# Kernel tuning notes

Hardware: AMD Instinct MI355X
Metric: run time of the kernel (lower is better)

The kernel has to match this reference:

```python
import jax, jax.numpy as jnp
import numpy as np

P = 16          # patch size (square)
HEADS = 8
DH = 64         # dim per head
SCALE = DH ** -0.5
EPS = 1e-5


def layernorm(x, g, b):
    mu = x.mean(-1, keepdims=True)
    var = ((x - mu) ** 2).mean(-1, keepdims=True)
    return (x - mu) * jax.lax.rsqrt(var + EPS) * g + b


def sattn(q, k, v):
    # q:[..., i, d], k/v:[..., j, d]; q already scaled
    sim = jnp.einsum('...id,...jd->...ij', q, k)
    a = jax.nn.softmax(sim, axis=-1)
    return jnp.einsum('...ij,...jd->...id', a, v)


def split_heads(t, b, N):
    return t.reshape(b, N, HEADS, DH).transpose(0, 2, 1, 3).reshape(b * HEADS, N, DH)


def merge_heads(t, b, N):
    return t.reshape(b, HEADS, N, DH).transpose(0, 2, 1, 3).reshape(b, N, HEADS * DH)


def qkv_cls(x, ln_g, ln_b, qkv_w):
    b, N, _ = x.shape
    xn = layernorm(x, ln_g, ln_b)
    q, k, v = jnp.split(xn @ qkv_w, 3, axis=-1)
    q = split_heads(q, b, N) * SCALE
    k = split_heads(k, b, N)
    v = split_heads(v, b, N)
    cls_out = sattn(q[:, :1], k, v)          # cls attends to everything
    return q[:, 1:], k[:, 1:], v[:, 1:], k[:, :1], v[:, :1], cls_out


def time_attention(x, ln_g, ln_b, qkv_w, out_w, out_b, f, n):
    b, N, _ = x.shape
    q_, k_, v_, cls_k, cls_v, cls_out = qkv_cls(x, ln_g, ln_b, qkv_w)
    bh = b * HEADS
    resh = lambda t: t.reshape(bh, f, n, DH).transpose(0, 2, 1, 3)  # 'b (f n) d -> (b n) f d' kept as [bh,n,f,d]
    q_, k_, v_ = resh(q_), resh(k_), resh(v_)
    ck = jnp.broadcast_to(cls_k[:, None], (bh, n, 1, DH))
    cv = jnp.broadcast_to(cls_v[:, None], (bh, n, 1, DH))
    out = sattn(q_, jnp.concatenate([ck, k_], 2), jnp.concatenate([cv, v_], 2))
    out = out.transpose(0, 2, 1, 3).reshape(bh, f * n, DH)
    out = jnp.concatenate([cls_out, out], axis=1)
    return merge_heads(out, b, N) @ out_w + out_b


def space_attention(x, ln_g, ln_b, qkv_w, out_w, out_b, f, n):
    b, N, _ = x.shape
    q_, k_, v_, cls_k, cls_v, cls_out = qkv_cls(x, ln_g, ln_b, qkv_w)
    bh = b * HEADS
    resh = lambda t: t.reshape(bh, f, n, DH)  # 'b (f n) d -> (b f) n d' kept as [bh,f,n,d]
    q_, k_, v_ = resh(q_), resh(k_), resh(v_)
    m = n // 2
    ck = jnp.broadcast_to(cls_k[:, None], (bh, f, 1, DH))
    cv = jnp.broadcast_to(cls_v[:, None], (bh, f, 1, DH))
    # mutual attention: first half queries attend to [cls, second half], and vice versa
    out1 = sattn(q_[:, :, :m], jnp.concatenate([ck, k_[:, :, m:]], 2), jnp.concatenate([cv, v_[:, :, m:]], 2))
    out2 = sattn(q_[:, :, m:], jnp.concatenate([ck, k_[:, :, :m]], 2), jnp.concatenate([cv, v_[:, :, :m]], 2))
    out = jnp.concatenate([out1, out2], axis=2).reshape(bh, f * n, DH)
    out = jnp.concatenate([cls_out, out], axis=1)
    return merge_heads(out, b, N) @ out_w + out_b


def geglu_ff(x, ln_g, ln_b, w1, b1, w2, b2):
    xn = layernorm(x, ln_g, ln_b)
    h = xn @ w1 + b1
    u, g = jnp.split(h, 2, axis=-1)
    return (u * jax.nn.gelu(g, approximate=False)) @ w2 + b2


def setup_inputs() -> dict:
    key = jax.random.key(0)
    ks = jax.random.split(key, 12)
    D, DEPTH, NC = 512, 12, 60
    inner = HEADS * DH
    B, F, C, H, W = 1, 4, 3, 480, 640
    n = (H // P) * (W // P)        # 1200
    N = F * n + 1                  # 4801
    pd = C * P * P                 # 768
    s = 0.02
    rn = lambda k, sh: jax.random.normal(k, sh, jnp.float32) * s
    z = lambda sh: jnp.zeros(sh, jnp.float32)
    o = lambda sh: jnp.ones(sh, jnp.float32)
    return {
        'video': jax.random.normal(ks[0], (B, F, C, H, W), jnp.float32),
        'patch_w': rn(ks[1], (pd, D)), 'patch_b': z((D,)),
        'pos_emb': rn(ks[2], (N, D)),
        'cls_token': rn(ks[3], (1, D)),
        't_ln_g': o((DEPTH, D)), 't_ln_b': z((DEPTH, D)),
        't_qkv_w': rn(ks[4], (DEPTH, D, 3 * inner)),
        't_out_w': rn(ks[5], (DEPTH, inner, D)), 't_out_b': z((DEPTH, D)),
        's_ln_g': o((DEPTH, D)), 's_ln_b': z((DEPTH, D)),
        's_qkv_w': rn(ks[6], (DEPTH, D, 3 * inner)),
        's_out_w': rn(ks[7], (DEPTH, inner, D)), 's_out_b': z((DEPTH, D)),
        'f_ln_g': o((DEPTH, D)), 'f_ln_b': z((DEPTH, D)),
        'f_w1': rn(ks[8], (DEPTH, D, 8 * D)), 'f_b1': z((DEPTH, 8 * D)),
        'f_w2': rn(ks[9], (DEPTH, 4 * D, D)), 'f_b2': z((DEPTH, D)),
        'o_ln_g': o((D,)), 'o_ln_b': z((D,)),
        'o_w': rn(ks[10], (D, NC)), 'o_b': z((NC,)),
    }


def reference(video, patch_w, patch_b, pos_emb, cls_token,
              t_ln_g, t_ln_b, t_qkv_w, t_out_w, t_out_b,
              s_ln_g, s_ln_b, s_qkv_w, s_out_w, s_out_b,
              f_ln_g, f_ln_b, f_w1, f_b1, f_w2, f_b2,
              o_ln_g, o_ln_b, o_w, o_b):
    b, f, c, H, W = video.shape
    hh, ww = H // P, W // P
    n = hh * ww
    wh = ww // 2
    half = W // 2

    def patchify(v):  # v: [b,f,c,H,W/2] -> [b, f*hh*wh, P*P*c]
        v = v.reshape(b, f, c, hh, P, wh, P)
        v = v.transpose(0, 1, 3, 5, 4, 6, 2)  # b f h w p1 p2 c
        return v.reshape(b, f * hh * wh, P * P * c)

    tok = jnp.concatenate([patchify(video[..., :half]), patchify(video[..., half:])], axis=1)
    tok = tok @ patch_w + patch_b
    x = jnp.concatenate([jnp.broadcast_to(cls_token[None], (b, 1, tok.shape[-1])), tok], axis=1)
    x = x + pos_emb[: x.shape[1]]

    depth = t_qkv_w.shape[0]
    for i in range(depth):
        x = time_attention(x, t_ln_g[i], t_ln_b[i], t_qkv_w[i], t_out_w[i], t_out_b[i], f, n) + x
        x = space_attention(x, s_ln_g[i], s_ln_b[i], s_qkv_w[i], s_out_w[i], s_out_b[i], f, n) + x
        x = geglu_ff(x, f_ln_g[i], f_ln_b[i], f_w1[i], f_b1[i], f_w2[i], f_b2[i]) + x

    cls = layernorm(x[:, 0], o_ln_g, o_ln_b)
    return cls @ o_w + o_b
```

## Files before the change

kernel.cpp:

```cpp
#include <hip/hip_runtime.h>
#include <cmath>


#define NT      4801
#define NP      4800
#define MP      4864
#define DM      512
#define QKV_ST  1536
#define LN_EPS  1e-5f
#define NCH     49

typedef __attribute__((ext_vector_type(8))) short bf16x8;
typedef __attribute__((ext_vector_type(4))) float f32x4;

__device__ __forceinline__ unsigned short f2b(float f) {
    union { float f; unsigned int u; } x; x.f = f;
    unsigned int r = (x.u + 0x7FFFu + ((x.u >> 16) & 1u)) >> 16;
    return (unsigned short)r;
}
__device__ __forceinline__ float b2f(unsigned short b) {
    union { unsigned int u; float f; } x; x.u = ((unsigned int)b) << 16;
    return x.f;
}
__device__ __forceinline__ unsigned int pack2(float a, float b) {
    return (unsigned int)f2b(a) | ((unsigned int)f2b(b) << 16);
}

__device__ __forceinline__ void gl_lds16(const void* g, void* l) {
    __builtin_amdgcn_global_load_lds(
        (__attribute__((address_space(1))) unsigned int*)(unsigned long long)(uintptr_t)g,
        (__attribute__((address_space(3))) unsigned int*)l, 16, 0, 0);
}

__global__ void patchify_kernel(const float* __restrict__ video, unsigned short* __restrict__ out)
{
    int idx = blockIdx.x * 256 + threadIdx.x;
    if (idx >= NP * 768) return;
    int tok = idx / 768, e = idx % 768;
    int c  = e % 3;
    int pe = e / 3;
    int p2 = pe % 16, p1 = pe / 16;
    int half = tok / 2400, r = tok % 2400;
    int f = r / 600, rr = r % 600;
    int hi = rr / 20, wi = rr % 20;
    int row = hi * 16 + p1;
    int col = half * 320 + wi * 16 + p2;
    out[idx] = f2b(video[(((size_t)f * 3 + c) * 480 + row) * 640 + col]);
}

__global__ void cls_init_kernel(const float* __restrict__ cls_token,
                                const float* __restrict__ pos, float* __restrict__ X)
{
    int d = blockIdx.x * 256 + threadIdx.x;
    if (d < DM) X[d] = cls_token[d] + pos[d];
}

__device__ __forceinline__ void transpose_tile(const float* __restrict__ in,
                                               unsigned short* __restrict__ out,
                                               int K, int N, int tile)
{
    __shared__ float T[32][33];
    int ntk = K / 32;
    int kt = tile % ntk, nt = tile / ntk;
    int k0 = kt * 32, n0 = nt * 32;
    int tx = threadIdx.x & 31, ty = threadIdx.x >> 5;
    #pragma unroll
    for (int i = 0; i < 4; i++)
        T[ty + 8 * i][tx] = in[(size_t)(k0 + ty + 8 * i) * N + n0 + tx];
    __syncthreads();
    #pragma unroll
    for (int i = 0; i < 4; i++)
        out[(size_t)(n0 + ty + 8 * i) * K + k0 + tx] = f2b(T[tx][ty + 8 * i]);
}

__global__ __launch_bounds__(256) void convertT_layer(
    const float* __restrict__ w0, const float* __restrict__ w1,
    const float* __restrict__ w2, const float* __restrict__ w3,
    const float* __restrict__ w4, const float* __restrict__ w5,
    unsigned short* __restrict__ out)
{
    int t = blockIdx.x;
    if      (t <  768) transpose_tile(w0, out + 0,       512, 1536, t);
    else if (t < 1024) transpose_tile(w1, out + 786432,  512,  512, t - 768);
    else if (t < 1792) transpose_tile(w2, out + 1048576, 512, 1536, t - 1024);
    else if (t < 2048) transpose_tile(w3, out + 1835008, 512,  512, t - 1792);
    else if (t < 4096) transpose_tile(w4, out + 2097152, 512, 4096, t - 2048);
    else               transpose_tile(w5, out + 4194304, 2048, 512, t - 4096);
}

__global__ __launch_bounds__(256) void convertT_one(
    const float* __restrict__ in, unsigned short* __restrict__ out, int K, int N)
{
    transpose_tile(in, out, K, N, blockIdx.x);
}

template<bool OB16>
__global__ __launch_bounds__(256, 4) void mfma_gemm(
    const unsigned short* __restrict__ A, const unsigned short* __restrict__ BT,
    const float* __restrict__ bias, const float* __restrict__ add,
    void* __restrict__ C, int Mv, int N, int K)
{
    __shared__ short Asm[128 * 64];
    __shared__ short Bsm[128 * 64];
    const int tid = threadIdx.x, w = tid >> 6, lane = tid & 63;
    const int row0 = blockIdx.y * 128, col0 = blockIdx.x * 128;
    const int wm = w >> 1, wn = w & 1;
    const int l15 = lane & 15, quad = lane >> 4;

    f32x4 acc[4][4] = {};

    int arows[4], aqs[4];
    #pragma unroll
    for (int i = 0; i < 4; i++) {
        int s = (w * 4 + i) * 64 + lane;
        arows[i] = s >> 3;
        aqs[i]   = (s & 7) ^ ((s >> 3) & 7);
    }

    for (int k0 = 0; k0 < K; k0 += 64) {
        __syncthreads();
        #pragma unroll
        for (int i = 0; i < 4; i++) {
            gl_lds16(A  + (size_t)(row0 + arows[i]) * K + k0 + aqs[i] * 8,
                     &Asm[(w * 4 + i) * 512]);
            gl_lds16(BT + (size_t)(col0 + arows[i]) * K + k0 + aqs[i] * 8,
                     &Bsm[(w * 4 + i) * 512]);
        }
        __syncthreads();
        #pragma unroll
        for (int ks = 0; ks < 2; ks++) {
            bf16x8 af[4], bfr[4];
            #pragma unroll
            for (int i = 0; i < 4; i++) {
                int m  = wm * 64 + i * 16 + l15;
                int pa = (ks * 4 + quad) ^ (m & 7);
                af[i]  = *(const bf16x8*)&Asm[m * 64 + pa * 8];
                int n  = wn * 64 + i * 16 + l15;
                int pb = (ks * 4 + quad) ^ (n & 7);
                bfr[i] = *(const bf16x8*)&Bsm[n * 64 + pb * 8];
            }
            #pragma unroll
            for (int i = 0; i < 4; i++)
                #pragma unroll
                for (int j = 0; j < 4; j++)
                    acc[i][j] = __builtin_amdgcn_mfma_f32_16x16x32_bf16(
                                    af[i], bfr[j], acc[i][j], 0, 0, 0);
        }
    }

    #pragma unroll
    for (int i = 0; i < 4; i++) {
        #pragma unroll
        for (int r = 0; r < 4; r++) {
            int row = row0 + wm * 64 + i * 16 + quad * 4 + r;
            if (row >= Mv) continue;
            #pragma unroll
            for (int j = 0; j < 4; j++) {
                int col = col0 + wn * 64 + j * 16 + l15;
                float v = acc[i][j][r];
                if (bias) v += bias[col];
                if (add)  v += add[(size_t)row * N + col];
                if (OB16) ((unsigned short*)C)[(size_t)row * N + col] = f2b(v);
                else      ((float*)C)[(size_t)row * N + col] = v;
            }
        }
    }
}

template<int SPLITS>
__global__ __launch_bounds__(256, 4) void mfma_gemm_sk(
    const unsigned short* __restrict__ A, const unsigned short* __restrict__ BT,
    const float* __restrict__ bias, float* __restrict__ C, int Mv, int N, int K)
{
    __shared__ short Asm[128 * 64];
    __shared__ short Bsm[128 * 64];
    const int tid = threadIdx.x, w = tid >> 6, lane = tid & 63;
    const int row0 = blockIdx.y * 128, col0 = blockIdx.x * 128;
    const int wm = w >> 1, wn = w & 1;
    const int l15 = lane & 15, quad = lane >> 4;
    const int kchunk = K / SPLITS;
    const int kbeg = blockIdx.z * kchunk;

    f32x4 acc[4][4] = {};

    int arows[4], aqs[4];
    #pragma unroll
    for (int i = 0; i < 4; i++) {
        int s = (w * 4 + i) * 64 + lane;
        arows[i] = s >> 3;
        aqs[i]   = (s & 7) ^ ((s >> 3) & 7);
    }

    for (int k0 = kbeg; k0 < kbeg + kchunk; k0 += 64) {
        __syncthreads();
        #pragma unroll
        for (int i = 0; i < 4; i++) {
            gl_lds16(A  + (size_t)(row0 + arows[i]) * K + k0 + aqs[i] * 8,
                     &Asm[(w * 4 + i) * 512]);
            gl_lds16(BT + (size_t)(col0 + arows[i]) * K + k0 + aqs[i] * 8,
                     &Bsm[(w * 4 + i) * 512]);
        }
        __syncthreads();
        #pragma unroll
        for (int ks = 0; ks < 2; ks++) {
            bf16x8 af[4], bfr[4];
            #pragma unroll
            for (int i = 0; i < 4; i++) {
                int m  = wm * 64 + i * 16 + l15;
                int pa = (ks * 4 + quad) ^ (m & 7);
                af[i]  = *(const bf16x8*)&Asm[m * 64 + pa * 8];
                int n  = wn * 64 + i * 16 + l15;
                int pb = (ks * 4 + quad) ^ (n & 7);
                bfr[i] = *(const bf16x8*)&Bsm[n * 64 + pb * 8];
            }
            #pragma unroll
            for (int i = 0; i < 4; i++)
                #pragma unroll
                for (int j = 0; j < 4; j++)
                    acc[i][j] = __builtin_amdgcn_mfma_f32_16x16x32_bf16(
                                    af[i], bfr[j], acc[i][j], 0, 0, 0);
        }
    }

    const bool addb = (blockIdx.z == 0) && (bias != nullptr);
    #pragma unroll
    for (int i = 0; i < 4; i++) {
        #pragma unroll
        for (int r = 0; r < 4; r++) {
            int row = row0 + wm * 64 + i * 16 + quad * 4 + r;
            if (row >= Mv) continue;
            #pragma unroll
            for (int j = 0; j < 4; j++) {
                int col = col0 + wn * 64 + j * 16 + l15;
                float v = acc[i][j][r];
                if (addb) v += bias[col];
                unsafeAtomicAdd(&C[(size_t)row * N + col], v);
            }
        }
    }
}

__global__ __launch_bounds__(256) void ln_bf16(
    const float* __restrict__ x, const float* __restrict__ g,
    const float* __restrict__ b, unsigned short* __restrict__ y, int M)
{
    int wid = threadIdx.x >> 6, lane = threadIdx.x & 63;
    int row = blockIdx.x * 4 + wid;
    if (row >= M) return;
    const float4* xr = (const float4*)(x + (size_t)row * DM);
    float4 v0 = xr[lane * 2], v1 = xr[lane * 2 + 1];
    float s  = v0.x + v0.y + v0.z + v0.w + v1.x + v1.y + v1.z + v1.w;
    float s2 = v0.x*v0.x + v0.y*v0.y + v0.z*v0.z + v0.w*v0.w
             + v1.x*v1.x + v1.y*v1.y + v1.z*v1.z + v1.w*v1.w;
    #pragma unroll
    for (int off = 32; off >= 1; off >>= 1) {
        s  += __shfl_xor(s, off);
        s2 += __shfl_xor(s2, off);
    }
    float mu = s * (1.f / DM);
    float var = s2 * (1.f / DM) - mu * mu;
    float r = rsqrtf(var + LN_EPS);
    const float4* gv = (const float4*)g;
    const float4* bv = (const float4*)b;
    unsigned int* yr = (unsigned int*)(y + (size_t)row * DM);
    #pragma unroll
    for (int i = 0; i < 2; i++) {
        float4 v = (i == 0) ? v0 : v1;
        float4 gg = gv[lane * 2 + i], bb = bv[lane * 2 + i];
        float ox = (v.x - mu) * r * gg.x + bb.x;
        float oy = (v.y - mu) * r * gg.y + bb.y;
        float oz = (v.z - mu) * r * gg.z + bb.z;
        float ow = (v.w - mu) * r * gg.w + bb.w;
        yr[lane * 4 + i * 2 + 0] = pack2(ox, oy);
        yr[lane * 4 + i * 2 + 1] = pack2(oz, ow);
    }
}

__global__ __launch_bounds__(256, 2) void time_attn(
    const unsigned short* __restrict__ qkv, unsigned short* __restrict__ out)
{
    int t = blockIdx.x * 256 + threadIdx.x;
    if (t >= 8 * NP) return;
    int h = t / NP, j = t - h * NP;
    int pos = j % 1200;
    union { bf16x8 v; unsigned short u[8]; } ld;
    float q[64];
    const unsigned short* qp = qkv + (size_t)(j + 1) * QKV_ST + h * 64;
    #pragma unroll
    for (int c = 0; c < 8; c++) {
        ld.v = *(const bf16x8*)(qp + c * 8);
        #pragma unroll
        for (int e = 0; e < 8; e++) q[c * 8 + e] = b2f(ld.u[e]) * 0.125f;
    }
    int rows[5] = {0, pos + 1, pos + 1201, pos + 2401, pos + 3601};
    float s[5];
    #pragma unroll
    for (int kk = 0; kk < 5; kk++) {
        const unsigned short* kp = qkv + (size_t)rows[kk] * QKV_ST + 512 + h * 64;
        float ss = 0.f;
        #pragma unroll
        for (int c = 0; c < 8; c++) {
            ld.v = *(const bf16x8*)(kp + c * 8);
            #pragma unroll
            for (int e = 0; e < 8; e++) ss += q[c * 8 + e] * b2f(ld.u[e]);
        }
        s[kk] = ss;
    }
    float mx = s[0];
    #pragma unroll
    for (int kk = 1; kk < 5; kk++) mx = fmaxf(mx, s[kk]);
    float e5[5], l = 0.f;
    #pragma unroll
    for (int kk = 0; kk < 5; kk++) { e5[kk] = __expf(s[kk] - mx); l += e5[kk]; }
    float rl = 1.f / l;
    float acc[64];
    #pragma unroll
    for (int d = 0; d < 64; d++) acc[d] = 0.f;
    #pragma unroll
    for (int kk = 0; kk < 5; kk++) {
        float p = e5[kk] * rl;
        const unsigned short* vp = qkv + (size_t)rows[kk] * QKV_ST + 1024 + h * 64;
        #pragma unroll
        for (int c = 0; c < 8; c++) {
            ld.v = *(const bf16x8*)(vp + c * 8);
            #pragma unroll
            for (int e = 0; e < 8; e++) acc[c * 8 + e] += p * b2f(ld.u[e]);
        }
    }
    unsigned int* op = (unsigned int*)(out + (size_t)(j + 1) * DM + h * 64);
    #pragma unroll
    for (int d2 = 0; d2 < 32; d2++) op[d2] = pack2(acc[2 * d2], acc[2 * d2 + 1]);
}

#define SPAD 72
__global__ __launch_bounds__(256, 2) void space_attn_mfma(
    const unsigned short* __restrict__ qkv, unsigned short* __restrict__ out)
{
    __shared__ short Ksm[64 * SPAD];
    __shared__ short VTsm[64 * SPAD];
    __shared__ short Psm[4][32 * SPAD];
    int qt = blockIdx.x, h = blockIdx.y, g = blockIdx.z;
    int f = g >> 1, half = g & 1;
    int tid = threadIdx.x, w = tid >> 6, lane = tid & 63;
    int l15 = lane & 15, quad = lane >> 4;

    int qrow_base = qt * 128 + w * 32;
    int qb = 1 + f * 1200 + half * 600;
    int kb = 1 + f * 1200 + (1 - half) * 600;

    bf16x8 aQ[2][2];
    #pragma unroll
    for (int mf = 0; mf < 2; mf++) {
        int qr = qrow_base + mf * 16 + l15;
        int qtok = qb + ((qr < 600) ? qr : 0);
        const unsigned short* qp = qkv + (size_t)qtok * QKV_ST + h * 64;
        #pragma unroll
        for (int ks = 0; ks < 2; ks++)
            aQ[mf][ks] = *(const bf16x8*)(qp + ks * 32 + quad * 8);
    }

    f32x4 O[2][4] = {};
    float mrow[2][4], lrow[2][4];
    #pragma unroll
    for (int mf = 0; mf < 2; mf++)
        #pragma unroll
        for (int r = 0; r < 4; r++) { mrow[mf][r] = -1e30f; lrow[mf][r] = 0.f; }

    for (int kt = 0; kt < 10; kt++) {
        __syncthreads();
        #pragma unroll
        for (int it = 0; it < 2; it++) {
            int c = tid + it * 256;
            int row = c >> 3, dc = (c & 7) * 8;
            int kidx = kt * 64 + row;
            int tok = (kidx == 0) ? 0 : ((kidx <= 600) ? kb + kidx - 1 : 0);
            const unsigned short* kp = qkv + (size_t)tok * QKV_ST + 512 + h * 64 + dc;
            *(bf16x8*)&Ksm[row * SPAD + dc] = *(const bf16x8*)kp;
            union { bf16x8 v; unsigned short u[8]; } vv;
            vv.v = *(const bf16x8*)(kp + 512);
            #pragma unroll
            for (int e = 0; e < 8; e++)
                VTsm[(dc + e) * SPAD + row] = vv.u[e];
        }
        __syncthreads();

        f32x4 S[2][4] = {};
        #pragma unroll
        for (int ks = 0; ks < 2; ks++) {
            bf16x8 bK[4];
            #pragma unroll
            for (int nf = 0; nf < 4; nf++)
                bK[nf] = *(const bf16x8*)&Ksm[(nf * 16 + l15) * SPAD + ks * 32 + quad * 8];
            #pragma unroll
            for (int mf = 0; mf < 2; mf++)
                #pragma unroll
                for (int nf = 0; nf < 4; nf++)
                    S[mf][nf] = __builtin_amdgcn_mfma_f32_16x16x32_bf16(
                                    aQ[mf][ks], bK[nf], S[mf][nf], 0, 0, 0);
        }

        #pragma unroll
        for (int mf = 0; mf < 2; mf++) {
            float pv[4][4];
            float lm[4] = {-1e30f, -1e30f, -1e30f, -1e30f};
            #pragma unroll
            for (int nf = 0; nf < 4; nf++) {
                int kidx = kt * 64 + nf * 16 + l15;
                bool valid = kidx <= 600;
                #pragma unroll
                for (int r = 0; r < 4; r++) {
                    float s = valid ? S[mf][nf][r] * 0.125f : -1e30f;
                    pv[nf][r] = s;
                    lm[r] = fmaxf(lm[r], s);
                }
            }
            #pragma unroll
            for (int off = 1; off < 16; off <<= 1)
                #pragma unroll
                for (int r = 0; r < 4; r++)
                    lm[r] = fmaxf(lm[r], __shfl_xor(lm[r], off));
            #pragma unroll
            for (int r = 0; r < 4; r++) {
                float nm = fmaxf(mrow[mf][r], lm[r]);
                float c = __expf(mrow[mf][r] - nm);
                mrow[mf][r] = nm;
                lrow[mf][r] *= c;
                #pragma unroll
                for (int nf = 0; nf < 4; nf++) O[mf][nf][r] *= c;
            }
            float rs[4] = {0.f, 0.f, 0.f, 0.f};
            #pragma unroll
            for (int nf = 0; nf < 4; nf++)
                #pragma unroll
                for (int r = 0; r < 4; r++) {
                    float p = __expf(pv[nf][r] - mrow[mf][r]);
                    pv[nf][r] = p;
                    rs[r] += p;
                }
            #pragma unroll
            for (int off = 1; off < 16; off <<= 1)
                #pragma unroll
                for (int r = 0; r < 4; r++)
                    rs[r] += __shfl_xor(rs[r], off);
            #pragma unroll
            for (int r = 0; r < 4; r++) lrow[mf][r] += rs[r];
            #pragma unroll
            for (int nf = 0; nf < 4; nf++)
                #pragma unroll
                for (int r = 0; r < 4; r++)
                    Psm[w][(mf * 16 + quad * 4 + r) * SPAD + nf * 16 + l15] = (short)f2b(pv[nf][r]);
        }
        asm volatile("s_waitcnt lgkmcnt(0)" ::: "memory");

        #pragma unroll
        for (int ks2 = 0; ks2 < 2; ks2++) {
            bf16x8 aP[2], bV[4];
            #pragma unroll
            for (int mf = 0; mf < 2; mf++)
                aP[mf] = *(const bf16x8*)&Psm[w][(mf * 16 + l15) * SPAD + ks2 * 32 + quad * 8];
            #pragma unroll
            for (int nf = 0; nf < 4; nf++)
                bV[nf] = *(const bf16x8*)&VTsm[(nf * 16 + l15) * SPAD + ks2 * 32 + quad * 8];
            #pragma unroll
            for (int mf = 0; mf < 2; mf++)
                #pragma unroll
                for (int nf = 0; nf < 4; nf++)
                    O[mf][nf] = __builtin_amdgcn_mfma_f32_16x16x32_bf16(
                                    aP[mf], bV[nf], O[mf][nf], 0, 0, 0);
        }
    }

    #pragma unroll
    for (int mf = 0; mf < 2; mf++)
        #pragma unroll
        for (int r = 0; r < 4; r++) {
            int qr = qrow_base + mf * 16 + quad * 4 + r;
            if (qr >= 600) continue;
            int qtok = qb + qr;
            float rl = 1.f / lrow[mf][r];
            #pragma unroll
            for (int nf = 0; nf < 4; nf++)
                out[(size_t)qtok * DM + h * 64 + nf * 16 + l15] = f2b(O[mf][nf][r] * rl);
        }
}

__global__ __launch_bounds__(256) void cls_attn_part(
    const unsigned short* __restrict__ qkv, float* __restrict__ part)
{
    int ch = blockIdx.x, h = blockIdx.y;
    int wid = threadIdx.x >> 6, lane = threadIdx.x & 63;
    __shared__ float sm[4], sl[4], sa[4][64];
    float qv = b2f(qkv[h * 64 + lane]) * 0.125f;
    int k0 = ch * 100 + wid * 25;
    float m = -1e30f, l = 0.f, acc = 0.f;
    for (int i = 0; i < 25; i += 2) {
        int key0 = k0 + i, key1 = key0 + 1;
        bool ok0 = key0 < NT;
        bool ok1 = (i + 1 < 25) && (key1 < NT);
        const unsigned short* kr0 = qkv + (size_t)(ok0 ? key0 : 0) * QKV_ST + 512 + h * 64;
        const unsigned short* kr1 = qkv + (size_t)(ok1 ? key1 : 0) * QKV_ST + 512 + h * 64;
        float s0 = qv * b2f(kr0[lane]);
        float v0 = b2f(kr0[512 + lane]);
        float s1 = qv * b2f(kr1[lane]);
        float v1 = b2f(kr1[512 + lane]);
        #pragma unroll
        for (int off = 32; off >= 1; off >>= 1) {
            s0 += __shfl_xor(s0, off);
            s1 += __shfl_xor(s1, off);
        }
        float nm = m;
        if (ok0) nm = fmaxf(nm, s0);
        if (ok1) nm = fmaxf(nm, s1);
        float c  = __expf(m - nm);
        float p0 = ok0 ? __expf(s0 - nm) : 0.f;
        float p1 = ok1 ? __expf(s1 - nm) : 0.f;
        l   = l * c + p0 + p1;
        acc = acc * c + p0 * v0 + p1 * v1;
        m = nm;
    }
    if (lane == 0) { sm[wid] = m; sl[wid] = l; }
    sa[wid][lane] = acc;
    __syncthreads();
    if (wid == 0) {
        float M2 = fmaxf(fmaxf(sm[0], sm[1]), fmaxf(sm[2], sm[3]));
        float L = 0.f, o = 0.f;
        #pragma unroll
        for (int w = 0; w < 4; w++) {
            float c = __expf(sm[w] - M2);
            L += sl[w] * c;
            o += sa[w][lane] * c;
        }
        float* p = part + ((size_t)h * NCH + ch) * 68;
        if (lane == 0) { p[0] = M2; p[1] = L; }
        p[4 + lane] = o;
    }
}

__global__ __launch_bounds__(64) void cls_attn_reduce(
    const float* __restrict__ part, unsigned short* __restrict__ out)
{
    int h = blockIdx.x, lane = threadIdx.x;
    float m = -1e30f, l = 0.f, acc = 0.f;
    for (int c = 0; c < NCH; c++) {
        const float* p = part + ((size_t)h * NCH + c) * 68;
        float cm = p[0], cl = p[1], ca = p[4 + lane];
        float nm = fmaxf(m, cm);
        float e1 = __expf(m - nm), e2 = __expf(cm - nm);
        l   = l * e1 + cl * e2;
        acc = acc * e1 + ca * e2;
        m = nm;
    }
    out[h * 64 + lane] = f2b(acc / l);
}

__global__ __launch_bounds__(256) void geglu_kernel(
    const unsigned short* __restrict__ h, unsigned short* __restrict__ out)
{
    int idx = blockIdx.x * 256 + threadIdx.x;
    if (idx >= NT * 256) return;
    int r = idx >> 8, cc = (idx & 255) * 8;
    const unsigned short* up = h + (size_t)r * 4096 + cc;
    const unsigned short* gp = up + 2048;
    float o[8];
    #pragma unroll
    for (int e = 0; e < 8; e++) {
        float u = b2f(up[e]), gg = b2f(gp[e]);
        o[e] = u * 0.5f * gg * (1.f + erff(gg * 0.70710678f));
    }
    unsigned int* op = (unsigned int*)(out + (size_t)r * 2048 + cc);
    #pragma unroll
    for (int e = 0; e < 4; e++) op[e] = pack2(o[2 * e], o[2 * e + 1]);
}

__global__ __launch_bounds__(64) void head_kernel(
    const float* __restrict__ x, const float* __restrict__ g,
    const float* __restrict__ b, const float* __restrict__ w,
    const float* __restrict__ ob, float* __restrict__ out)
{
    __shared__ float xn[DM];
    int lane = threadIdx.x;
    const float4* xr = (const float4*)x;
    float4 v0 = xr[lane * 2], v1 = xr[lane * 2 + 1];
    float s  = v0.x + v0.y + v0.z + v0.w + v1.x + v1.y + v1.z + v1.w;
    float s2 = v0.x*v0.x + v0.y*v0.y + v0.z*v0.z + v0.w*v0.w
             + v1.x*v1.x + v1.y*v1.y + v1.z*v1.z + v1.w*v1.w;
    #pragma unroll
    for (int off = 32; off >= 1; off >>= 1) {
        s  += __shfl_xor(s, off);
        s2 += __shfl_xor(s2, off);
    }
    float mu = s * (1.f / DM);
    float var = s2 * (1.f / DM) - mu * mu;
    float r = rsqrtf(var + LN_EPS);
    #pragma unroll
    for (int i = 0; i < 8; i++) {
        int d = lane * 8 + i;
        xn[d] = (x[d] - mu) * r * g[d] + b[d];
    }
    __syncthreads();
    if (lane < 60) {
        float a = ob[lane];
        for (int d = 0; d < DM; d++) a += xn[d] * w[d * 60 + lane];
        out[lane] = a;
    }
}

extern "C" void kernel_launch(void* const* d_in, const int* in_sizes, int n_in,
                              void* d_out, int out_size, void* d_ws, size_t ws_size,
                              hipStream_t stream)
{
    const float* video     = (const float*)d_in[0];
    const float* patch_w   = (const float*)d_in[1];
    const float* patch_b   = (const float*)d_in[2];
    const float* pos_emb   = (const float*)d_in[3];
    const float* cls_token = (const float*)d_in[4];
    const float* t_ln_g    = (const float*)d_in[5];
    const float* t_ln_b    = (const float*)d_in[6];
    const float* t_qkv_w   = (const float*)d_in[7];
    const float* t_out_w   = (const float*)d_in[8];
    const float* t_out_b   = (const float*)d_in[9];
    const float* s_ln_g    = (const float*)d_in[10];
    const float* s_ln_b    = (const float*)d_in[11];
    const float* s_qkv_w   = (const float*)d_in[12];
    const float* s_out_w   = (const float*)d_in[13];
    const float* s_out_b   = (const float*)d_in[14];
    const float* f_ln_g    = (const float*)d_in[15];
    const float* f_ln_b    = (const float*)d_in[16];
    const float* f_w1      = (const float*)d_in[17];
    const float* f_b1      = (const float*)d_in[18];
    const float* f_w2      = (const float*)d_in[19];
    const float* f_b2      = (const float*)d_in[20];
    const float* o_ln_g    = (const float*)d_in[21];
    const float* o_ln_b    = (const float*)d_in[22];
    const float* o_w       = (const float*)d_in[23];
    const float* o_b       = (const float*)d_in[24];

    char* ws = (char*)d_ws;
    size_t o = 0;
    float*          X    = (float*)(ws + o);          o += (size_t)(MP + 1) * 512 * 4;
    unsigned short* XN   = (unsigned short*)(ws + o); o += (size_t)MP * 512 * 2;
    unsigned short* QKV  = (unsigned short*)(ws + o); o += (size_t)MP * 1536 * 2;
    unsigned short* H16  = (unsigned short*)(ws + o); o += (size_t)MP * 4096 * 2;
    unsigned short* MID  = (unsigned short*)(ws + o); o += (size_t)MP * 2048 * 2;
    unsigned short* PT   = (unsigned short*)(ws + o); o += (size_t)MP * 768 * 2;
    unsigned short* W16  = (unsigned short*)(ws + o); o += (size_t)5242880 * 2;
    unsigned short* PW16 = (unsigned short*)(ws + o); o += (size_t)512 * 768 * 2;
    float*          CP   = (float*)(ws + o);          o += (size_t)8 * NCH * 68 * 4;

    patchify_kernel<<<(NP * 768 + 255) / 256, 256, 0, stream>>>(video, PT);
    cls_init_kernel<<<2, 256, 0, stream>>>(cls_token, pos_emb, X);
    convertT_one<<<(768 / 32) * (512 / 32), 256, 0, stream>>>(patch_w, PW16, 768, 512);
    mfma_gemm<false><<<dim3(4, 38), 256, 0, stream>>>(PT, PW16, patch_b, pos_emb + DM,
                                                      X + DM, NP, DM, 768);

    dim3 g_qkv(12, 38), g_ff1(32, 38);
    dim3 g_out_sk(4, 38, 2), g_ff2_sk(4, 38, 4);
    for (int i = 0; i < 12; i++) {
        convertT_layer<<<5120, 256, 0, stream>>>(
            t_qkv_w + (size_t)i * 512 * 1536, t_out_w + (size_t)i * 512 * 512,
            s_qkv_w + (size_t)i * 512 * 1536, s_out_w + (size_t)i * 512 * 512,
            f_w1 + (size_t)i * 512 * 4096, f_w2 + (size_t)i * 2048 * 512, W16);

        ln_bf16<<<1201, 256, 0, stream>>>(X, t_ln_g + i * DM, t_ln_b + i * DM, XN, NT);
        mfma_gemm<true><<<g_qkv, 256, 0, stream>>>(XN, W16 + 0, nullptr, nullptr,
                                                   QKV, NT, QKV_ST, DM);
        time_attn<<<150, 256, 0, stream>>>(QKV, MID);
        cls_attn_part<<<dim3(NCH, 8), 256, 0, stream>>>(QKV, CP);
        cls_attn_reduce<<<8, 64, 0, stream>>>(CP, MID);
        mfma_gemm_sk<2><<<g_out_sk, 256, 0, stream>>>(MID, W16 + 786432, t_out_b + i * DM,
                                                      X, NT, DM, DM);
        ln_bf16<<<1201, 256, 0, stream>>>(X, s_ln_g + i * DM, s_ln_b + i * DM, XN, NT);
        mfma_gemm<true><<<g_qkv, 256, 0, stream>>>(XN, W16 + 1048576, nullptr, nullptr,
                                                   QKV, NT, QKV_ST, DM);
        space_attn_mfma<<<dim3(5, 8, 8), 256, 0, stream>>>(QKV, MID);
        cls_attn_part<<<dim3(NCH, 8), 256, 0, stream>>>(QKV, CP);
        cls_attn_reduce<<<8, 64, 0, stream>>>(CP, MID);
        mfma_gemm_sk<2><<<g_out_sk, 256, 0, stream>>>(MID, W16 + 1835008, s_out_b + i * DM,
                                                      X, NT, DM, DM);
        ln_bf16<<<1201, 256, 0, stream>>>(X, f_ln_g + i * DM, f_ln_b + i * DM, XN, NT);
        mfma_gemm<true><<<g_ff1, 256, 0, stream>>>(XN, W16 + 2097152, f_b1 + i * 4096,
                                                   nullptr, H16, NT, 4096, DM);
        geglu_kernel<<<(NT * 256 + 255) / 256, 256, 0, stream>>>(H16, MID);
        mfma_gemm_sk<4><<<g_ff2_sk, 256, 0, stream>>>(MID, W16 + 4194304, f_b2 + i * DM,
                                                      X, NT, DM, 2048);
    }

    head_kernel<<<1, 64, 0, stream>>>(X, o_ln_g, o_ln_b, o_w, o_b, (float*)d_out);
}
```

Before: 4.474 ms.

## Double-buffer LDS tiles in MFMA GEMM kernels to overlap loads with compute

Both the plain and split-K bf16 MFMA GEMM kernels now keep two LDS buffers for the A and B tiles. The next K-tile is prefetched with direct global-to-LDS loads while MFMAs run on the current tile, and one wait plus barrier per iteration replaces the two syncthreads. This is meant to hide global memory latency behind compute. In exchange LDS use doubles to 64KB per block and the occupancy hint drops from 4 to 2 blocks per CU, so there is less latency hiding from other resident waves.

```diff
diff --git a/kernel.cpp b/kernel.cpp
--- a/kernel.cpp
+++ b/kernel.cpp
@@ -95,13 +95,13 @@
 }
 
 template<bool OB16>
-__global__ __launch_bounds__(256, 4) void mfma_gemm(
+__global__ __launch_bounds__(256, 2) void mfma_gemm(
     const unsigned short* __restrict__ A, const unsigned short* __restrict__ BT,
     const float* __restrict__ bias, const float* __restrict__ add,
     void* __restrict__ C, int Mv, int N, int K)
 {
-    __shared__ short Asm[128 * 64];
-    __shared__ short Bsm[128 * 64];
+    __shared__ short Asm[2][128 * 64];
+    __shared__ short Bsm[2][128 * 64];
     const int tid = threadIdx.x, w = tid >> 6, lane = tid & 63;
     const int row0 = blockIdx.y * 128, col0 = blockIdx.x * 128;
     const int wm = w >> 1, wn = w & 1;
@@ -116,17 +116,33 @@
         arows[i] = s >> 3;
         aqs[i]   = (s & 7) ^ ((s >> 3) & 7);
     }
-
-    for (int k0 = 0; k0 < K; k0 += 64) {
-        __syncthreads();
-        #pragma unroll
-        for (int i = 0; i < 4; i++) {
-            gl_lds16(A  + (size_t)(row0 + arows[i]) * K + k0 + aqs[i] * 8,
-                     &Asm[(w * 4 + i) * 512]);
-            gl_lds16(BT + (size_t)(col0 + arows[i]) * K + k0 + aqs[i] * 8,
-                     &Bsm[(w * 4 + i) * 512]);
-        }
-        __syncthreads();
+    const unsigned short* Ab = A  + (size_t)row0 * K;
+    const unsigned short* Bb = BT + (size_t)col0 * K;
+
+    #pragma unroll
+    for (int i = 0; i < 4; i++) {
+        gl_lds16(Ab + (size_t)arows[i] * K + aqs[i] * 8, &Asm[0][(w * 4 + i) * 512]);
+        gl_lds16(Bb + (size_t)arows[i] * K + aqs[i] * 8, &Bsm[0][(w * 4 + i) * 512]);
+    }
+    asm volatile("s_waitcnt vmcnt(0)" ::: "memory");
+    __builtin_amdgcn_s_barrier();
+
+    const int nt = K >> 6;
+    int cur = 0;
+    for (int t = 0; t < nt; t++) {
+        if (t + 1 < nt) {
+            const int k0 = (t + 1) << 6;
+            #pragma unroll
+            for (int i = 0; i < 4; i++) {
+                gl_lds16(Ab + (size_t)arows[i] * K + k0 + aqs[i] * 8,
+                         &Asm[cur ^ 1][(w * 4 + i) * 512]);
+                gl_lds16(Bb + (size_t)arows[i] * K + k0 + aqs[i] * 8,
+                         &Bsm[cur ^ 1][(w * 4 + i) * 512]);
+            }
+        }
+        __builtin_amdgcn_sched_barrier(0);
+        const short* As = Asm[cur];
+        const short* Bs = Bsm[cur];
         #pragma unroll
         for (int ks = 0; ks < 2; ks++) {
             bf16x8 af[4], bfr[4];
@@ -134,10 +150,10 @@
             for (int i = 0; i < 4; i++) {
                 int m  = wm * 64 + i * 16 + l15;
                 int pa = (ks * 4 + quad) ^ (m & 7);
-                af[i]  = *(const bf16x8*)&Asm[m * 64 + pa * 8];
+                af[i]  = *(const bf16x8*)&As[m * 64 + pa * 8];
                 int n  = wn * 64 + i * 16 + l15;
                 int pb = (ks * 4 + quad) ^ (n & 7);
-                bfr[i] = *(const bf16x8*)&Bsm[n * 64 + pb * 8];
+                bfr[i] = *(const bf16x8*)&Bs[n * 64 + pb * 8];
             }
             #pragma unroll
             for (int i = 0; i < 4; i++)
@@ -146,6 +162,9 @@
                     acc[i][j] = __builtin_amdgcn_mfma_f32_16x16x32_bf16(
                                     af[i], bfr[j], acc[i][j], 0, 0, 0);
         }
+        asm volatile("s_waitcnt vmcnt(0)" ::: "memory");
+        __builtin_amdgcn_s_barrier();
+        cur ^= 1;
     }
 
     #pragma unroll
@@ -168,12 +187,12 @@
 }
 
 template<int SPLITS>
-__global__ __launch_bounds__(256, 4) void mfma_gemm_sk(
+__global__ __launch_bounds__(256, 2) void mfma_gemm_sk(
     const unsigned short* __restrict__ A, const unsigned short* __restrict__ BT,
     const float* __restrict__ bias, float* __restrict__ C, int Mv, int N, int K)
 {
-    __shared__ short Asm[128 * 64];
-    __shared__ short Bsm[128 * 64];
+    __shared__ short Asm[2][128 * 64];
+    __shared__ short Bsm[2][128 * 64];
     const int tid = threadIdx.x, w = tid >> 6, lane = tid & 63;
     const int row0 = blockIdx.y * 128, col0 = blockIdx.x * 128;
     const int wm = w >> 1, wn = w & 1;
@@ -190,17 +209,33 @@
         arows[i] = s >> 3;
         aqs[i]   = (s & 7) ^ ((s >> 3) & 7);
     }
-
-    for (int k0 = kbeg; k0 < kbeg + kchunk; k0 += 64) {
-        __syncthreads();
-        #pragma unroll
-        for (int i = 0; i < 4; i++) {
-            gl_lds16(A  + (size_t)(row0 + arows[i]) * K + k0 + aqs[i] * 8,
-                     &Asm[(w * 4 + i) * 512]);
-            gl_lds16(BT + (size_t)(col0 + arows[i]) * K + k0 + aqs[i] * 8,
-                     &Bsm[(w * 4 + i) * 512]);
-        }
-        __syncthreads();
+    const unsigned short* Ab = A  + (size_t)row0 * K + kbeg;
+    const unsigned short* Bb = BT + (size_t)col0 * K + kbeg;
+
+    #pragma unroll
+    for (int i = 0; i < 4; i++) {
+        gl_lds16(Ab + (size_t)arows[i] * K + aqs[i] * 8, &Asm[0][(w * 4 + i) * 512]);
+        gl_lds16(Bb + (size_t)arows[i] * K + aqs[i] * 8, &Bsm[0][(w * 4 + i) * 512]);
+    }
+    asm volatile("s_waitcnt vmcnt(0)" ::: "memory");
+    __builtin_amdgcn_s_barrier();
+
+    const int nt = kchunk >> 6;
+    int cur = 0;
+    for (int t = 0; t < nt; t++) {
+        if (t + 1 < nt) {
+            const int k0 = (t + 1) << 6;
+            #pragma unroll
+            for (int i = 0; i < 4; i++) {
+                gl_lds16(Ab + (size_t)arows[i] * K + k0 + aqs[i] * 8,
+                         &Asm[cur ^ 1][(w * 4 + i) * 512]);
+                gl_lds16(Bb + (size_t)arows[i] * K + k0 + aqs[i] * 8,
+                         &Bsm[cur ^ 1][(w * 4 + i) * 512]);
+            }
+        }
+        __builtin_amdgcn_sched_barrier(0);
+        const short* As = Asm[cur];
+        const short* Bs = Bsm[cur];
         #pragma unroll
         for (int ks = 0; ks < 2; ks++) {
             bf16x8 af[4], bfr[4];
@@ -208,10 +243,10 @@
             for (int i = 0; i < 4; i++) {
                 int m  = wm * 64 + i * 16 + l15;
                 int pa = (ks * 4 + quad) ^ (m & 7);
-                af[i]  = *(const bf16x8*)&Asm[m * 64 + pa * 8];
+                af[i]  = *(const bf16x8*)&As[m * 64 + pa * 8];
                 int n  = wn * 64 + i * 16 + l15;
                 int pb = (ks * 4 + quad) ^ (n & 7);
-                bfr[i] = *(const bf16x8*)&Bsm[n * 64 + pb * 8];
+                bfr[i] = *(const bf16x8*)&Bs[n * 64 + pb * 8];
             }
             #pragma unroll
             for (int i = 0; i < 4; i++)
@@ -220,6 +255,9 @@
                     acc[i][j] = __builtin_amdgcn_mfma_f32_16x16x32_bf16(
                                     af[i], bfr[j], acc[i][j], 0, 0, 0);
         }
+        asm volatile("s_waitcnt vmcnt(0)" ::: "memory");
+        __builtin_amdgcn_s_barrier();
+        cur ^= 1;
     }
 
     const bool addb = (blockIdx.z == 0) && (bias != nullptr);
```

New measurement: 4.653 ms. 1.04x slower.
